# Optimization experiments

Hardware: AMD Instinct MI355X
Metric: run time of the kernel (lower is better)

The kernel has to match this reference:

```python
import jax, jax.numpy as jnp
import numpy as np

QUERY_DIM = 3072
HEADS = 24
HEAD_DIM = 128
INNER = HEADS * HEAD_DIM  # 3072
MLP_HIDDEN = int(QUERY_DIM * 4.0)  # 12288
MLP_MULT = 2
EPS = 1e-5
B, S = 1, 4096


def setup_inputs() -> dict:
    key = jax.random.key(0)
    ks = jax.random.split(key, 8)
    hidden_states = jax.random.normal(ks[0], (B, S, QUERY_DIM), dtype=jnp.float32)
    # rotary angles for half the head dim (interleaved / non-neox style)
    t = jnp.arange(S, dtype=jnp.float32)[:, None]
    inv_freq = 1.0 / (10000.0 ** (jnp.arange(0, HEAD_DIM, 2, dtype=jnp.float32) / HEAD_DIM))
    ang = t * inv_freq[None, :]
    cos = jnp.cos(ang)
    sin = jnp.sin(ang)
    W_qkv_mlp = jax.random.normal(ks[1], (QUERY_DIM, 3 * INNER + MLP_HIDDEN * MLP_MULT), dtype=jnp.float32) * 0.02
    W_out = jax.random.normal(ks[2], (INNER + MLP_HIDDEN, QUERY_DIM), dtype=jnp.float32) * 0.02
    b_out = jnp.zeros((QUERY_DIM,), dtype=jnp.float32)
    norm_q_w = jnp.ones((HEAD_DIM,), dtype=jnp.float32)
    norm_k_w = jnp.ones((HEAD_DIM,), dtype=jnp.float32)
    return {"hidden_states": hidden_states, "cos": cos, "sin": sin,
            "W_qkv_mlp": W_qkv_mlp, "W_out": W_out, "b_out": b_out,
            "norm_q_w": norm_q_w, "norm_k_w": norm_k_w}


def _rmsnorm(x, w, eps=EPS):
    var = jnp.mean(jnp.square(x), axis=-1, keepdims=True)
    return x * jax.lax.rsqrt(var + eps) * w


def _rope_interleaved(x, cos, sin):
    # x: [B,S,H,D]; cos/sin: [S, D//2]. Non-neox: rotate interleaved pairs.
    x1 = x[..., 0::2]
    x2 = x[..., 1::2]
    c = cos[None, :, None, :]
    s = sin[None, :, None, :]
    o1 = x1 * c - x2 * s
    o2 = x2 * c + x1 * s
    return jnp.stack([o1, o2], axis=-1).reshape(x.shape)


def reference(hidden_states, cos, sin, W_qkv_mlp, W_out, b_out, norm_q_w, norm_k_w):
    h = hidden_states @ W_qkv_mlp  # [B,S, 3*INNER + 2*MLP_HIDDEN]
    qkv, mlp = jnp.split(h, [3 * INNER], axis=-1)
    q, k, v = jnp.split(qkv, 3, axis=-1)
    q = q.reshape(B, S, HEADS, HEAD_DIM)
    k = k.reshape(B, S, HEADS, HEAD_DIM)
    v = v.reshape(B, S, HEADS, HEAD_DIM)
    q = _rmsnorm(q, norm_q_w)
    k = _rmsnorm(k, norm_k_w)
    q = _rope_interleaved(q, cos, sin)
    k = _rope_interleaved(k, cos, sin)
    scale = 1.0 / np.sqrt(HEAD_DIM)
    scores = jnp.einsum('bqhd,bkhd->bhqk', q, k) * scale
    probs = jax.nn.softmax(scores, axis=-1)
    attn = jnp.einsum('bhqk,bkhd->bqhd', probs, v)
    attn = attn.reshape(B, S, INNER)
    m1, m2 = jnp.split(mlp, 2, axis=-1)
    mlp_out = jax.nn.silu(m1) * m2
    out = jnp.concatenate([attn, mlp_out], axis=-1) @ W_out + b_out
    return out
```

## Files before the change

kernel.cpp:

```cpp
#include <hip/hip_runtime.h>

typedef short shortx8 __attribute__((ext_vector_type(8)));
typedef float floatx4 __attribute__((ext_vector_type(4)));
typedef unsigned short u16;

#define GLB(x) ((const __attribute__((address_space(1))) void*)(x))
#define LDSC(x) ((__attribute__((address_space(3))) void*)(x))

__device__ __forceinline__ float bf2f(u16 u) {
  unsigned x = ((unsigned)u) << 16;
  float f;
  __builtin_memcpy(&f, &x, 4);
  return f;
}
__device__ __forceinline__ u16 f2bf(float f) {
  unsigned x;
  __builtin_memcpy(&x, &f, 4);
  x += 0x7fffu + ((x >> 16) & 1u);
  return (u16)(x >> 16);
}

__global__ __launch_bounds__(256) void cast_bf16(const float* __restrict__ src,
                                                 u16* __restrict__ dst) {
  const size_t i = ((size_t)blockIdx.x * 256 + threadIdx.x) << 3;
  floatx4 a = *(const floatx4*)(src + i);
  floatx4 b = *(const floatx4*)(src + i + 4);
  shortx8 o;
#pragma unroll
  for (int e = 0; e < 4; ++e) {
    o[e] = (short)f2bf(a[e]);
    o[e + 4] = (short)f2bf(b[e]);
  }
  *(shortx8*)(dst + i) = o;
}

__global__ __launch_bounds__(256) void transpose_cast(const float* __restrict__ src,
                                                      u16* __restrict__ dst,
                                                      int R, int C) {
  __shared__ u16 T[64 * 72];
  const int tiles_c = C >> 6;
  const int r0 = (blockIdx.x / tiles_c) << 6;
  const int c0 = (blockIdx.x % tiles_c) << 6;
  const int tid = threadIdx.x;
  const int rl = tid >> 4;
  const int cb = (tid & 15) << 2;
#pragma unroll
  for (int rr = 0; rr < 4; ++rr) {
    const int row = rr * 16 + rl;
    floatx4 v = *(const floatx4*)(src + (size_t)(r0 + row) * C + c0 + cb);
#pragma unroll
    for (int i = 0; i < 4; ++i) T[(cb + i) * 72 + row] = f2bf(v[i]);
  }
  __syncthreads();
#pragma unroll
  for (int ii = 0; ii < 2; ++ii) {
    const int chunk = tid + (ii << 8);
    const int cr = chunk >> 3;
    const int r8 = (chunk & 7) << 3;
    shortx8 v = *(const shortx8*)(T + cr * 72 + r8);
    *(shortx8*)(dst + (size_t)(c0 + cr) * R + r0 + r8) = v;
  }
}

#define BAR() asm volatile("s_barrier" ::: "memory")
#define WAITV8() asm volatile("s_waitcnt vmcnt(8)" ::: "memory")

template <int OUT32>
__global__ __launch_bounds__(512, 2) void gemm8(const u16* __restrict__ A,
                                                const u16* __restrict__ B,
                                                void* __restrict__ Cout,
                                                const float* __restrict__ bias,
                                                int M, int N, int K) {
  __shared__ u16 lds[8 * 8192];

  const int nbm = M >> 8;
  const int nwg = nbm * (N >> 8);
  const int cpx = nwg >> 3;
  const int wg = ((int)blockIdx.x & 7) * cpx + ((int)blockIdx.x >> 3);
  const int bm = wg % nbm;
  const int bn = wg / nbm;

  const int tid = threadIdx.x;
  const int lane = tid & 63;
  const int w = tid >> 6;
  const int wm = w >> 2;
  const int wn = w & 3;
  const int l15 = lane & 15;
  const int l4 = lane >> 4;
  const int NT = K >> 6;

  const int lrow = lane >> 2;
  const int lblk = lane & 3;

#define UNIT(buf, mat, ks) (lds + (((buf) * 4 + (mat) * 2 + (ks)) << 13))

  const u16* Abase = A + (size_t)bm * 256 * K;
  const u16* Bbase = B + (size_t)bn * 256 * K;

  auto STAGE = [&](int mat, int ks, int buf, int t) {
    const u16* gb = mat ? Bbase : Abase;
#pragma unroll
    for (int j = 0; j < 2; ++j) {
      const int row = (w * 2 + j) * 16 + lrow;
      const int sblk = lblk ^ ((row >> 1) & 3);
      const u16* src = gb + (size_t)row * K + (t << 6) + (ks << 5) + (sblk << 3);
      __builtin_amdgcn_global_load_lds(GLB(src),
                                       LDSC(UNIT(buf, mat, ks) + ((w * 2 + j) << 9)),
                                       16, 0, 0);
    }
  };
  auto LDA = [&](int mf, int ks, int buf) -> shortx8 {
    const int row = wm * 128 + mf * 16 + l15;
    return *(const shortx8*)(UNIT(buf, 0, ks) + row * 32 + ((l4 ^ ((row >> 1) & 3)) << 3));
  };
  auto LDB = [&](int nf, int ks, int buf) -> shortx8 {
    const int row = wn * 64 + nf * 16 + l15;
    return *(const shortx8*)(UNIT(buf, 1, ks) + row * 32 + ((l4 ^ ((row >> 1) & 3)) << 3));
  };

  floatx4 acc[8][4] = {};

  STAGE(0, 0, 0, 0); STAGE(1, 0, 0, 0);
  STAGE(0, 1, 0, 0); STAGE(1, 1, 0, 0);
  STAGE(0, 0, 1, 1); STAGE(1, 0, 1, 1);
  WAITV8();
  BAR();

  for (int T = 0; T < NT; ++T) {
    const int cur = T & 1, nxt = cur ^ 1;
    const int t1 = (T + 1 < NT) ? T + 1 : NT - 1;
    const int t2 = (T + 2 < NT) ? T + 2 : NT - 1;
    shortx8 af[4], bf[4];

#pragma unroll
    for (int m = 0; m < 4; ++m) af[m] = LDA(m, 0, cur);
#pragma unroll
    for (int n = 0; n < 4; ++n) bf[n] = LDB(n, 0, cur);
    STAGE(0, 1, nxt, t1);
    BAR();
    __builtin_amdgcn_s_setprio(1);
#pragma unroll
    for (int m = 0; m < 4; ++m)
#pragma unroll
      for (int n = 0; n < 4; ++n)
        acc[m][n] = __builtin_amdgcn_mfma_f32_16x16x32_bf16(af[m], bf[n], acc[m][n], 0, 0, 0);
    __builtin_amdgcn_s_setprio(0);
    BAR();

#pragma unroll
    for (int m = 0; m < 4; ++m) af[m] = LDA(4 + m, 0, cur);
    STAGE(1, 1, nxt, t1);
    BAR();
    __builtin_amdgcn_s_setprio(1);
#pragma unroll
    for (int m = 0; m < 4; ++m)
#pragma unroll
      for (int n = 0; n < 4; ++n)
        acc[4 + m][n] = __builtin_amdgcn_mfma_f32_16x16x32_bf16(af[m], bf[n], acc[4 + m][n], 0, 0, 0);
    __builtin_amdgcn_s_setprio(0);
    WAITV8();
    BAR();

#pragma unroll
    for (int m = 0; m < 4; ++m) af[m] = LDA(m, 1, cur);
#pragma unroll
    for (int n = 0; n < 4; ++n) bf[n] = LDB(n, 1, cur);
    STAGE(0, 0, cur, t2);
    BAR();
    __builtin_amdgcn_s_setprio(1);
#pragma unroll
    for (int m = 0; m < 4; ++m)
#pragma unroll
      for (int n = 0; n < 4; ++n)
        acc[m][n] = __builtin_amdgcn_mfma_f32_16x16x32_bf16(af[m], bf[n], acc[m][n], 0, 0, 0);
    __builtin_amdgcn_s_setprio(0);
    BAR();

#pragma unroll
    for (int m = 0; m < 4; ++m) af[m] = LDA(4 + m, 1, cur);
    STAGE(1, 0, cur, t2);
    BAR();
    __builtin_amdgcn_s_setprio(1);
#pragma unroll
    for (int m = 0; m < 4; ++m)
#pragma unroll
      for (int n = 0; n < 4; ++n)
        acc[4 + m][n] = __builtin_amdgcn_mfma_f32_16x16x32_bf16(af[m], bf[n], acc[4 + m][n], 0, 0, 0);
    __builtin_amdgcn_s_setprio(0);
    WAITV8();
    BAR();
  }

  const int orow0 = bm * 256 + wm * 128 + (l4 << 2);
  const int ocol0 = bn * 256 + wn * 64 + l15;
  if (OUT32) {
    float* C = (float*)Cout;
    float bv[4];
#pragma unroll
    for (int n = 0; n < 4; ++n) bv[n] = bias[ocol0 + n * 16];
#pragma unroll
    for (int m = 0; m < 8; ++m)
#pragma unroll
      for (int n = 0; n < 4; ++n)
#pragma unroll
        for (int r = 0; r < 4; ++r)
          C[(size_t)(orow0 + m * 16 + r) * N + ocol0 + n * 16] = acc[m][n][r] + bv[n];
  } else {
    u16* C = (u16*)Cout;
#pragma unroll
    for (int m = 0; m < 8; ++m)
#pragma unroll
      for (int n = 0; n < 4; ++n)
#pragma unroll
        for (int r = 0; r < 4; ++r)
          C[(size_t)(orow0 + m * 16 + r) * N + ocol0 + n * 16] = f2bf(acc[m][n][r]);
  }
}
#undef UNIT

#define QSCALE (0.08838834764831845f * 1.4426950408889634f)

__global__ __launch_bounds__(256, 2) void qkv_prep(
    const u16* __restrict__ H, const float* __restrict__ cosb,
    const float* __restrict__ sinb, const float* __restrict__ nqw,
    const float* __restrict__ nkw, u16* __restrict__ Qo, u16* __restrict__ Ko,
    u16* __restrict__ Vo) {
  __shared__ u16 VT[128 * 72];
  const int head = blockIdx.y;
  const int t0 = blockIdx.x << 6;
  const int tid = threadIdx.x;
  const int tl = tid >> 2;
  const int db = (tid & 3) << 5;
  const int token = t0 + tl;

  const u16* hp = H + (size_t)token * 33792 + head * 128 + db;
  shortx8 qv[4], kvv[4], vv[4];
#pragma unroll
  for (int i = 0; i < 4; ++i) {
    qv[i] = *(const shortx8*)(hp + i * 8);
    kvv[i] = *(const shortx8*)(hp + 3072 + i * 8);
    vv[i] = *(const shortx8*)(hp + 6144 + i * 8);
  }
  float qx[32], kx[32];
  float sq = 0.f, sk = 0.f;
#pragma unroll
  for (int i = 0; i < 4; ++i)
#pragma unroll
    for (int j = 0; j < 8; ++j) {
      float a = bf2f((u16)qv[i][j]); qx[i * 8 + j] = a; sq += a * a;
      float b = bf2f((u16)kvv[i][j]); kx[i * 8 + j] = b; sk += b * b;
    }
  sq += __shfl_xor(sq, 1); sq += __shfl_xor(sq, 2);
  sk += __shfl_xor(sk, 1); sk += __shfl_xor(sk, 2);
  const float rq = rsqrtf(sq * (1.0f / 128.0f) + 1e-5f);
  const float rk = rsqrtf(sk * (1.0f / 128.0f) + 1e-5f);

  shortx8 oqv[4], okv[4];
#pragma unroll
  for (int p = 0; p < 16; ++p) {
    const float c = cosb[(size_t)token * 64 + (db >> 1) + p];
    const float s = sinb[(size_t)token * 64 + (db >> 1) + p];
    const int vi = p >> 2, vj = (p & 3) << 1;
    float a1 = qx[2 * p] * rq * nqw[db + 2 * p];
    float a2 = qx[2 * p + 1] * rq * nqw[db + 2 * p + 1];
    oqv[vi][vj] = (short)f2bf((a1 * c - a2 * s) * QSCALE);
    oqv[vi][vj + 1] = (short)f2bf((a2 * c + a1 * s) * QSCALE);
    float b1 = kx[2 * p] * rk * nkw[db + 2 * p];
    float b2 = kx[2 * p + 1] * rk * nkw[db + 2 * p + 1];
    okv[vi][vj] = (short)f2bf(b1 * c - b2 * s);
    okv[vi][vj + 1] = (short)f2bf(b2 * c + b1 * s);
  }
  {
    u16* qo = Qo + (size_t)head * 4096 * 128 + (size_t)token * 128 + db;
    u16* ko = Ko + (size_t)head * 4096 * 128 + (size_t)token * 128 + db;
#pragma unroll
    for (int i = 0; i < 4; ++i) {
      *(shortx8*)(qo + i * 8) = oqv[i];
      *(shortx8*)(ko + i * 8) = okv[i];
    }
  }
#pragma unroll
  for (int i = 0; i < 4; ++i)
#pragma unroll
    for (int j = 0; j < 8; ++j) VT[(db + i * 8 + j) * 72 + tl] = (u16)vv[i][j];
  __syncthreads();
#pragma unroll
  for (int ii = 0; ii < 4; ++ii) {
    const int chunk = tid + (ii << 8);
    const int d = chunk >> 3;
    const int j8 = (chunk & 7) << 3;
    shortx8 v = *(const shortx8*)(VT + d * 72 + j8);
    *(shortx8*)(Vo + (size_t)head * 128 * 4096 + (size_t)d * 4096 + t0 + j8) = v;
  }
}

__global__ __launch_bounds__(256) void mlp_act(const u16* __restrict__ H,
                                               u16* __restrict__ CC) {
  const size_t id = (size_t)blockIdx.x * 256 + threadIdx.x;
  const int t = (int)(id / 1536);
  const int j = ((int)(id % 1536)) << 3;
  const u16* base = H + (size_t)t * 33792;
  shortx8 a = *(const shortx8*)(base + 9216 + j);
  shortx8 b = *(const shortx8*)(base + 21504 + j);
  shortx8 o;
#pragma unroll
  for (int e = 0; e < 8; ++e) {
    float x = bf2f((u16)a[e]);
    float y = bf2f((u16)b[e]);
    float sg = 1.0f / (1.0f + exp2f(-1.4426950408889634f * x));
    o[e] = (short)f2bf(x * sg * y);
  }
  *(shortx8*)(CC + (size_t)t * 15360 + 3072 + j) = o;
}

__global__ __launch_bounds__(256, 2) void attn_kernel(const u16* __restrict__ Qg,
                                                      const u16* __restrict__ Kg,
                                                      const u16* __restrict__ Vg,
                                                      u16* __restrict__ CC) {
  __shared__ u16 Ks[64 * 128];
  __shared__ u16 Vs[128 * 64];
  __shared__ u16 Ps[4 * 16 * 64];

  const int head = blockIdx.y;
  const int q0 = blockIdx.x << 6;
  const int tid = threadIdx.x;
  const int lane = tid & 63;
  const int wave = tid >> 6;
  const int l15 = lane & 15;
  const int l4 = lane >> 4;

  const u16* Qh = Qg + (size_t)head * 4096 * 128;
  const u16* Kh = Kg + (size_t)head * 4096 * 128;
  const u16* Vh = Vg + (size_t)head * 128 * 4096;

  shortx8 qf[4];
  {
    const u16* qp = Qh + (size_t)(q0 + wave * 16 + l15) * 128 + l4 * 8;
#pragma unroll
    for (int ks = 0; ks < 4; ++ks) qf[ks] = *(const shortx8*)(qp + ks * 32);
  }

  floatx4 o[8] = {};
  float mrun[4], lrun[4];
#pragma unroll
  for (int r = 0; r < 4; ++r) { mrun[r] = -1e30f; lrun[r] = 0.0f; }

  u16* Pw = Ps + wave * 1024;
  const int swz = l15 & 7;

  for (int s0 = 0; s0 < 4096; s0 += 64) {
    if (wave < 2) {
#pragma unroll
      for (int i = 0; i < 8; ++i) {
        const int c = wave * 8 + i;
        const int row = c * 4 + (lane >> 4);
        const int blk = (lane & 15) ^ (row & 7);
        __builtin_amdgcn_global_load_lds(GLB(Kh + (size_t)(s0 + row) * 128 + blk * 8),
                                         LDSC(Ks + c * 512), 16, 0, 0);
      }
    } else {
#pragma unroll
      for (int i = 0; i < 8; ++i) {
        const int cc = (wave - 2) * 8 + i;
        const int row = cc * 8 + (lane >> 3);
        const int blk = (lane & 7) ^ (row & 7);
        __builtin_amdgcn_global_load_lds(GLB(Vh + (size_t)row * 4096 + s0 + blk * 8),
                                         LDSC(Vs + cc * 512), 16, 0, 0);
      }
    }
    __syncthreads();

    floatx4 s[4] = {};
#pragma unroll
    for (int n = 0; n < 4; ++n) {
      const int krow = n * 16 + l15;
#pragma unroll
      for (int ks = 0; ks < 4; ++ks) {
        shortx8 kf = *(const shortx8*)(Ks + krow * 128 + (((ks * 4 + l4) ^ swz) << 3));
        s[n] = __builtin_amdgcn_mfma_f32_16x16x32_bf16(qf[ks], kf, s[n], 0, 0, 0);
      }
    }

    float alpha[4];
#pragma unroll
    for (int r = 0; r < 4; ++r) {
      float v = fmaxf(fmaxf(s[0][r], s[1][r]), fmaxf(s[2][r], s[3][r]));
      v = fmaxf(v, __shfl_xor(v, 1));
      v = fmaxf(v, __shfl_xor(v, 2));
      v = fmaxf(v, __shfl_xor(v, 4));
      v = fmaxf(v, __shfl_xor(v, 8));
      const float mn = fmaxf(mrun[r], v);
      alpha[r] = exp2f(mrun[r] - mn);
      mrun[r] = mn;
    }

    float rs[4] = {0.f, 0.f, 0.f, 0.f};
#pragma unroll
    for (int n = 0; n < 4; ++n) {
#pragma unroll
      for (int r = 0; r < 4; ++r) {
        const float p = exp2f(s[n][r] - mrun[r]);
        rs[r] += p;
        const int prow = (l4 << 2) + r;
        const int pblk = ((n << 1) + (l15 >> 3)) ^ (prow & 7);
        Pw[prow * 64 + (pblk << 3) + (l15 & 7)] = f2bf(p);
      }
    }
#pragma unroll
    for (int r = 0; r < 4; ++r) {
      float v = rs[r];
      v += __shfl_xor(v, 1);
      v += __shfl_xor(v, 2);
      v += __shfl_xor(v, 4);
      v += __shfl_xor(v, 8);
      lrun[r] = lrun[r] * alpha[r] + v;
    }
#pragma unroll
    for (int nd = 0; nd < 8; ++nd)
#pragma unroll
      for (int r = 0; r < 4; ++r) o[nd][r] *= alpha[r];

    shortx8 pf[2];
#pragma unroll
    for (int ks = 0; ks < 2; ++ks)
      pf[ks] = *(const shortx8*)(Pw + l15 * 64 + (((ks * 4 + l4) ^ swz) << 3));
#pragma unroll
    for (int nd = 0; nd < 8; ++nd) {
      const int vrow = nd * 16 + l15;
#pragma unroll
      for (int ks = 0; ks < 2; ++ks) {
        shortx8 vf = *(const shortx8*)(Vs + vrow * 64 + (((ks * 4 + l4) ^ swz) << 3));
        o[nd] = __builtin_amdgcn_mfma_f32_16x16x32_bf16(pf[ks], vf, o[nd], 0, 0, 0);
      }
    }
    __syncthreads();
  }

#pragma unroll
  for (int r = 0; r < 4; ++r) {
    const float inv = 1.0f / lrun[r];
    const int row = q0 + wave * 16 + (l4 << 2) + r;
    u16* outp = CC + (size_t)row * 15360 + head * 128 + l15;
#pragma unroll
    for (int nd = 0; nd < 8; ++nd) outp[nd << 4] = f2bf(o[nd][r] * inv);
  }
}

extern "C" void kernel_launch(void* const* d_in, const int* in_sizes, int n_in,
                              void* d_out, int out_size, void* d_ws, size_t ws_size,
                              hipStream_t stream) {
  const float* hs = (const float*)d_in[0];
  const float* cosb = (const float*)d_in[1];
  const float* sinb = (const float*)d_in[2];
  const float* w1 = (const float*)d_in[3];
  const float* wout = (const float*)d_in[4];
  const float* bout = (const float*)d_in[5];
  const float* nqw = (const float*)d_in[6];
  const float* nkw = (const float*)d_in[7];
  float* out = (float*)d_out;

  char* ws = (char*)d_ws;
  u16* X16 = (u16*)ws; ws += (size_t)4096 * 3072 * 2;
  u16* W1T = (u16*)ws; ws += (size_t)33792 * 3072 * 2;
  u16* WOT = (u16*)ws; ws += (size_t)3072 * 15360 * 2;
  u16* H   = (u16*)ws; ws += (size_t)4096 * 33792 * 2;
  u16* Qb  = (u16*)ws; ws += (size_t)24 * 4096 * 128 * 2;
  u16* Kb  = (u16*)ws; ws += (size_t)24 * 4096 * 128 * 2;
  u16* VTb = (u16*)ws; ws += (size_t)24 * 4096 * 128 * 2;
  u16* CC  = (u16*)ws; ws += (size_t)4096 * 15360 * 2;

  cast_bf16<<<6144, 256, 0, stream>>>(hs, X16);
  transpose_cast<<<(3072 / 64) * (33792 / 64), 256, 0, stream>>>(w1, W1T, 3072, 33792);
  transpose_cast<<<(15360 / 64) * (3072 / 64), 256, 0, stream>>>(wout, WOT, 15360, 3072);
  gemm8<0><<<(4096 / 256) * (33792 / 256), 512, 0, stream>>>(X16, W1T, H, nullptr,
                                                             4096, 33792, 3072);
  qkv_prep<<<dim3(64, 24), 256, 0, stream>>>(H, cosb, sinb, nqw, nkw, Qb, Kb, VTb);
  mlp_act<<<(4096 * 12288 / 8) / 256, 256, 0, stream>>>(H, CC);
  attn_kernel<<<dim3(64, 24), 256, 0, stream>>>(Qb, Kb, VTb, CC);
  gemm8<1><<<(4096 / 256) * (3072 / 256), 512, 0, stream>>>(CC, WOT, out, bout,
                                                            4096, 3072, 15360);
}
```

Baseline: 1.995 ms.

## Double-buffer K/V tiles in attention kernel with async prefetch

The attention kernel now keeps two LDS buffers for K and V and issues the global-to-LDS loads for the next 64-key tile before computing on the current one. All four waves share the loading instead of splitting K and V between wave pairs, and the trailing __syncthreads is replaced by a vmcnt(0) wait plus a barrier at the top of each iteration. MFMA sections are also wrapped in s_setprio. The goal is to hide K/V load latency behind compute, at the cost of doubling the K/V LDS footprint (about 66KB per block), which may limit how many blocks fit per CU.

```diff
diff --git a/kernel.cpp b/kernel.cpp
--- a/kernel.cpp
+++ b/kernel.cpp
@@ -6,6 +6,9 @@
 
 #define GLB(x) ((const __attribute__((address_space(1))) void*)(x))
 #define LDSC(x) ((__attribute__((address_space(3))) void*)(x))
+#define BAR() asm volatile("s_barrier" ::: "memory")
+#define WAITV8() asm volatile("s_waitcnt vmcnt(8)" ::: "memory")
+#define WAITV0() asm volatile("s_waitcnt vmcnt(0)" ::: "memory")
 
 __device__ __forceinline__ float bf2f(u16 u) {
   unsigned x = ((unsigned)u) << 16;
@@ -61,9 +64,6 @@
     *(shortx8*)(dst + (size_t)(c0 + cr) * R + r0 + r8) = v;
   }
 }
-
-#define BAR() asm volatile("s_barrier" ::: "memory")
-#define WAITV8() asm volatile("s_waitcnt vmcnt(8)" ::: "memory")
 
 template <int OUT32>
 __global__ __launch_bounds__(512, 2) void gemm8(const u16* __restrict__ A,
@@ -317,8 +317,8 @@
                                                       const u16* __restrict__ Kg,
                                                       const u16* __restrict__ Vg,
                                                       u16* __restrict__ CC) {
-  __shared__ u16 Ks[64 * 128];
-  __shared__ u16 Vs[128 * 64];
+  __shared__ u16 Ks[2][64 * 128];
+  __shared__ u16 Vs[2][128 * 64];
   __shared__ u16 Ps[4 * 16 * 64];
 
   const int head = blockIdx.y;
@@ -333,6 +333,25 @@
   const u16* Kh = Kg + (size_t)head * 4096 * 128;
   const u16* Vh = Vg + (size_t)head * 128 * 4096;
 
+  auto STAGE_KV = [&](int s0, int buf) {
+#pragma unroll
+    for (int i = 0; i < 4; ++i) {
+      const int c = wave * 4 + i;
+      const int row = c * 4 + (lane >> 4);
+      const int blk = (lane & 15) ^ (row & 7);
+      __builtin_amdgcn_global_load_lds(GLB(Kh + (size_t)(s0 + row) * 128 + blk * 8),
+                                       LDSC(&Ks[buf][c * 512]), 16, 0, 0);
+    }
+#pragma unroll
+    for (int i = 0; i < 4; ++i) {
+      const int cc = wave * 4 + i;
+      const int row = cc * 8 + (lane >> 3);
+      const int blk = (lane & 7) ^ (row & 7);
+      __builtin_amdgcn_global_load_lds(GLB(Vh + (size_t)row * 4096 + s0 + blk * 8),
+                                       LDSC(&Vs[buf][cc * 512]), 16, 0, 0);
+    }
+  };
+
   shortx8 qf[4];
   {
     const u16* qp = Qh + (size_t)(q0 + wave * 16 + l15) * 128 + l4 * 8;
@@ -348,38 +367,26 @@
   u16* Pw = Ps + wave * 1024;
   const int swz = l15 & 7;
 
-  for (int s0 = 0; s0 < 4096; s0 += 64) {
-    if (wave < 2) {
-#pragma unroll
-      for (int i = 0; i < 8; ++i) {
-        const int c = wave * 8 + i;
-        const int row = c * 4 + (lane >> 4);
-        const int blk = (lane & 15) ^ (row & 7);
-        __builtin_amdgcn_global_load_lds(GLB(Kh + (size_t)(s0 + row) * 128 + blk * 8),
-                                         LDSC(Ks + c * 512), 16, 0, 0);
-      }
-    } else {
-#pragma unroll
-      for (int i = 0; i < 8; ++i) {
-        const int cc = (wave - 2) * 8 + i;
-        const int row = cc * 8 + (lane >> 3);
-        const int blk = (lane & 7) ^ (row & 7);
-        __builtin_amdgcn_global_load_lds(GLB(Vh + (size_t)row * 4096 + s0 + blk * 8),
-                                         LDSC(Vs + cc * 512), 16, 0, 0);
-      }
-    }
-    __syncthreads();
+  STAGE_KV(0, 0);
+
+  for (int it = 0; it < 64; ++it) {
+    const int cur = it & 1;
+    WAITV0();
+    BAR();
+    if (it < 63) STAGE_KV((it + 1) << 6, cur ^ 1);
 
     floatx4 s[4] = {};
+    __builtin_amdgcn_s_setprio(1);
 #pragma unroll
     for (int n = 0; n < 4; ++n) {
       const int krow = n * 16 + l15;
 #pragma unroll
       for (int ks = 0; ks < 4; ++ks) {
-        shortx8 kf = *(const shortx8*)(Ks + krow * 128 + (((ks * 4 + l4) ^ swz) << 3));
+        shortx8 kf = *(const shortx8*)(&Ks[cur][krow * 128 + (((ks * 4 + l4) ^ swz) << 3)]);
         s[n] = __builtin_amdgcn_mfma_f32_16x16x32_bf16(qf[ks], kf, s[n], 0, 0, 0);
       }
     }
+    __builtin_amdgcn_s_setprio(0);
 
     float alpha[4];
 #pragma unroll
@@ -424,16 +431,17 @@
 #pragma unroll
     for (int ks = 0; ks < 2; ++ks)
       pf[ks] = *(const shortx8*)(Pw + l15 * 64 + (((ks * 4 + l4) ^ swz) << 3));
+    __builtin_amdgcn_s_setprio(1);
 #pragma unroll
     for (int nd = 0; nd < 8; ++nd) {
       const int vrow = nd * 16 + l15;
 #pragma unroll
       for (int ks = 0; ks < 2; ++ks) {
-        shortx8 vf = *(const shortx8*)(Vs + vrow * 64 + (((ks * 4 + l4) ^ swz) << 3));
+        shortx8 vf = *(const shortx8*)(&Vs[cur][vrow * 64 + (((ks * 4 + l4) ^ swz) << 3)]);
         o[nd] = __builtin_amdgcn_mfma_f32_16x16x32_bf16(pf[ks], vf, o[nd], 0, 0, 0);
       }
     }
-    __syncthreads();
+    __builtin_amdgcn_s_setprio(0);
   }
 
 #pragma unroll
```

Result: no change. 2.028 ms (+1.6%).

## Split-K the output projection GEMM and skip no-op rescale in attention

Applied to the files above, without the earlier changes.

The output GEMM (4096x3072, K=15360) used only 192 workgroups, which underfills the GPU. It is now split four ways along K via blockIdx.y, giving 768 workgroups. Each slice writes fp32 partials into the reused H buffer, and a separate reduce kernel sums the partials and adds the bias. The attention loop also skips the O rescale when every alpha in the wavefront equals 1. This trades extra partial-sum traffic and one more launch for better occupancy.

```diff
diff --git a/kernel.cpp b/kernel.cpp
--- a/kernel.cpp
+++ b/kernel.cpp
@@ -6,6 +6,8 @@
 
 #define GLB(x) ((const __attribute__((address_space(1))) void*)(x))
 #define LDSC(x) ((__attribute__((address_space(3))) void*)(x))
+#define BAR() asm volatile("s_barrier" ::: "memory")
+#define WAITV8() asm volatile("s_waitcnt vmcnt(8)" ::: "memory")
 
 __device__ __forceinline__ float bf2f(u16 u) {
   unsigned x = ((unsigned)u) << 16;
@@ -62,15 +64,11 @@
   }
 }
 
-#define BAR() asm volatile("s_barrier" ::: "memory")
-#define WAITV8() asm volatile("s_waitcnt vmcnt(8)" ::: "memory")
-
-template <int OUT32>
+template <int MODE>
 __global__ __launch_bounds__(512, 2) void gemm8(const u16* __restrict__ A,
                                                 const u16* __restrict__ B,
                                                 void* __restrict__ Cout,
-                                                const float* __restrict__ bias,
-                                                int M, int N, int K) {
+                                                int M, int N, int K, int Ksub) {
   __shared__ u16 lds[8 * 8192];
 
   const int nbm = M >> 8;
@@ -79,6 +77,7 @@
   const int wg = ((int)blockIdx.x & 7) * cpx + ((int)blockIdx.x >> 3);
   const int bm = wg % nbm;
   const int bn = wg / nbm;
+  const int koff = (int)blockIdx.y * Ksub;
 
   const int tid = threadIdx.x;
   const int lane = tid & 63;
@@ -87,15 +86,15 @@
   const int wn = w & 3;
   const int l15 = lane & 15;
   const int l4 = lane >> 4;
-  const int NT = K >> 6;
+  const int NT = Ksub >> 6;
 
   const int lrow = lane >> 2;
   const int lblk = lane & 3;
 
 #define UNIT(buf, mat, ks) (lds + (((buf) * 4 + (mat) * 2 + (ks)) << 13))
 
-  const u16* Abase = A + (size_t)bm * 256 * K;
-  const u16* Bbase = B + (size_t)bn * 256 * K;
+  const u16* Abase = A + (size_t)bm * 256 * K + koff;
+  const u16* Bbase = B + (size_t)bn * 256 * K + koff;
 
   auto STAGE = [&](int mat, int ks, int buf, int t) {
     const u16* gb = mat ? Bbase : Abase;
@@ -193,19 +192,7 @@
 
   const int orow0 = bm * 256 + wm * 128 + (l4 << 2);
   const int ocol0 = bn * 256 + wn * 64 + l15;
-  if (OUT32) {
-    float* C = (float*)Cout;
-    float bv[4];
-#pragma unroll
-    for (int n = 0; n < 4; ++n) bv[n] = bias[ocol0 + n * 16];
-#pragma unroll
-    for (int m = 0; m < 8; ++m)
-#pragma unroll
-      for (int n = 0; n < 4; ++n)
-#pragma unroll
-        for (int r = 0; r < 4; ++r)
-          C[(size_t)(orow0 + m * 16 + r) * N + ocol0 + n * 16] = acc[m][n][r] + bv[n];
-  } else {
+  if (MODE == 0) {
     u16* C = (u16*)Cout;
 #pragma unroll
     for (int m = 0; m < 8; ++m)
@@ -214,9 +201,31 @@
 #pragma unroll
         for (int r = 0; r < 4; ++r)
           C[(size_t)(orow0 + m * 16 + r) * N + ocol0 + n * 16] = f2bf(acc[m][n][r]);
+  } else {
+    float* C = (float*)Cout + (size_t)blockIdx.y * M * N;
+#pragma unroll
+    for (int m = 0; m < 8; ++m)
+#pragma unroll
+      for (int n = 0; n < 4; ++n)
+#pragma unroll
+        for (int r = 0; r < 4; ++r)
+          C[(size_t)(orow0 + m * 16 + r) * N + ocol0 + n * 16] = acc[m][n][r];
   }
 }
 #undef UNIT
+
+__global__ __launch_bounds__(256) void reduce_bias(const float* __restrict__ P,
+                                                   const float* __restrict__ bias,
+                                                   float* __restrict__ out) {
+  const size_t base = ((size_t)blockIdx.x * 256 + threadIdx.x) << 2;
+  const size_t stride = (size_t)4096 * 3072;
+  floatx4 a = *(const floatx4*)(P + base);
+  floatx4 b = *(const floatx4*)(P + stride + base);
+  floatx4 c = *(const floatx4*)(P + 2 * stride + base);
+  floatx4 d = *(const floatx4*)(P + 3 * stride + base);
+  floatx4 bb = *(const floatx4*)(bias + (base % 3072));
+  *(floatx4*)(out + base) = a + b + c + d + bb;
+}
 
 #define QSCALE (0.08838834764831845f * 1.4426950408889634f)
 
@@ -415,10 +424,13 @@
       v += __shfl_xor(v, 8);
       lrun[r] = lrun[r] * alpha[r] + v;
     }
-#pragma unroll
-    for (int nd = 0; nd < 8; ++nd)
-#pragma unroll
-      for (int r = 0; r < 4; ++r) o[nd][r] *= alpha[r];
+    if (__any((alpha[0] < 1.0f) || (alpha[1] < 1.0f) ||
+              (alpha[2] < 1.0f) || (alpha[3] < 1.0f))) {
+#pragma unroll
+      for (int nd = 0; nd < 8; ++nd)
+#pragma unroll
+        for (int r = 0; r < 4; ++r) o[nd][r] *= alpha[r];
+    }
 
     shortx8 pf[2];
 #pragma unroll
@@ -468,15 +480,17 @@
   u16* Kb  = (u16*)ws; ws += (size_t)24 * 4096 * 128 * 2;
   u16* VTb = (u16*)ws; ws += (size_t)24 * 4096 * 128 * 2;
   u16* CC  = (u16*)ws; ws += (size_t)4096 * 15360 * 2;
+  float* Pk = (float*)H;
 
   cast_bf16<<<6144, 256, 0, stream>>>(hs, X16);
   transpose_cast<<<(3072 / 64) * (33792 / 64), 256, 0, stream>>>(w1, W1T, 3072, 33792);
   transpose_cast<<<(15360 / 64) * (3072 / 64), 256, 0, stream>>>(wout, WOT, 15360, 3072);
-  gemm8<0><<<(4096 / 256) * (33792 / 256), 512, 0, stream>>>(X16, W1T, H, nullptr,
-                                                             4096, 33792, 3072);
+  gemm8<0><<<(4096 / 256) * (33792 / 256), 512, 0, stream>>>(X16, W1T, H,
+                                                             4096, 33792, 3072, 3072);
   qkv_prep<<<dim3(64, 24), 256, 0, stream>>>(H, cosb, sinb, nqw, nkw, Qb, Kb, VTb);
   mlp_act<<<(4096 * 12288 / 8) / 256, 256, 0, stream>>>(H, CC);
   attn_kernel<<<dim3(64, 24), 256, 0, stream>>>(Qb, Kb, VTb, CC);
-  gemm8<1><<<(4096 / 256) * (3072 / 256), 512, 0, stream>>>(CC, WOT, out, bout,
-                                                            4096, 3072, 15360);
-}
+  gemm8<1><<<dim3((4096 / 256) * (3072 / 256), 4), 512, 0, stream>>>(
+      CC, WOT, Pk, 4096, 3072, 15360, 3840);
+  reduce_bias<<<(4096 * 3072 / 4) / 256, 256, 0, stream>>>(Pk, bout, out);
+}
```

Result: no change. 2.001 ms (+0.3%).
